# Performance work log

Hardware: AMD Instinct MI355X
Metric: run time of the kernel (lower is better)

## Reference

```python
import jax, jax.numpy as jnp
from jax import lax
import numpy as np

B, S, D, H2, V = 1024, 256, 128, 5, 50257
EPS = 1e-5


def setup_inputs() -> dict:
    key = jax.random.key(0)
    ks = jax.random.split(key, 12)
    s = 0.08  # init scale ~ 1/sqrt(D)
    return {
        "x": jax.random.randint(ks[0], (B, S), 0, V),
        "emb": jax.random.normal(ks[1], (V, D), jnp.float32) * s,
        "W_ih1": jax.random.normal(ks[2], (D, D), jnp.float32) * s,
        "b_ih1": jax.random.normal(ks[3], (D,), jnp.float32) * s,
        "W_hh1": jax.random.normal(ks[4], (D, D), jnp.float32) * s,
        "b_hh1": jax.random.normal(ks[5], (D,), jnp.float32) * s,
        "g1": jnp.ones((D,), jnp.float32),
        "be1": jnp.zeros((D,), jnp.float32),
        "W_ih2": jax.random.normal(ks[6], (H2, D), jnp.float32) * s,
        "b_ih2": jax.random.normal(ks[7], (H2,), jnp.float32) * s,
        "W_hh2": jax.random.normal(ks[8], (H2, H2), jnp.float32) * s,
        "b_hh2": jax.random.normal(ks[9], (H2,), jnp.float32) * s,
        "g2": jnp.ones((H2,), jnp.float32),
        "be2": jnp.zeros((H2,), jnp.float32),
    }


def _rnn(xproj, W_hh):
    """Vanilla tanh RNN. xproj: [B,S,H] = x @ W_ih^T + b_ih + b_hh (precomputed)."""
    h0 = jnp.zeros((xproj.shape[0], W_hh.shape[0]), xproj.dtype)

    def step(h, xt):  # xt: [B,H]
        h = jnp.tanh(xt + h @ W_hh.T)
        return h, h

    _, hs = lax.scan(step, h0, jnp.swapaxes(xproj, 0, 1))  # [S,B,H]
    return jnp.swapaxes(hs, 0, 1)  # [B,S,H]


def _ln(z, g, b):
    m = jnp.mean(z, axis=-1, keepdims=True)
    v = jnp.mean(jnp.square(z - m), axis=-1, keepdims=True)
    return (z - m) * lax.rsqrt(v + EPS) * g + b


def reference(x, emb, W_ih1, b_ih1, W_hh1, b_hh1, g1, be1,
              W_ih2, b_ih2, W_hh2, b_hh2, g2, be2):
    e = emb[x]  # [B,S,D]
    z = _rnn(e @ W_ih1.T + (b_ih1 + b_hh1), W_hh1)
    z = _ln(z, g1, be1)
    z = _rnn(z @ W_ih2.T + (b_ih2 + b_hh2), W_hh2)  # [B,S,5]
    z = _ln(z, g2, be2)
    pooled = jnp.mean(z, axis=1)  # AvgPool1d over full seq -> [B,5]
    return jax.nn.softmax(pooled, axis=1)
```

## Files before the change

### kernel.cpp

```cpp
#include <hip/hip_runtime.h>
#include <stdint.h>

#define S_LEN 256
#define DIM   128
#define EPSL  1e-5f

typedef __bf16 bf16x8 __attribute__((ext_vector_type(8)));
typedef float  f32x4  __attribute__((ext_vector_type(4)));

__device__ __forceinline__ unsigned short f2bf_bits(float f) {
  union { float f; unsigned int u; } v; v.f = f;
  unsigned int r = v.u + 0x7fffu + ((v.u >> 16) & 1u);
  return (unsigned short)(r >> 16);
}
__device__ __forceinline__ float bf2f_bits(unsigned short b) {
  union { float f; unsigned int u; } v; v.u = ((unsigned int)b) << 16; return v.f;
}
__device__ __forceinline__ unsigned f2bf_rhu(float f) {
  return (__float_as_uint(f) + 0x8000u) >> 16;
}
__device__ __forceinline__ unsigned pack_rhu(float lo, float hi) {
  return __builtin_amdgcn_perm(__float_as_uint(hi) + 0x8000u,
                               __float_as_uint(lo) + 0x8000u, 0x07060302u);
}
__device__ __forceinline__ float tanh_fast(float x) {
  float e = __expf(2.f * x);
  return 1.f - 2.f * __builtin_amdgcn_rcpf(e + 1.f);
}

template<int CTRL>
__device__ __forceinline__ float dpp_rot_add(float v) {
  int r = __builtin_amdgcn_update_dpp(0, __float_as_int(v), CTRL, 0xF, 0xF, true);
  return v + __int_as_float(r);
}
template<int CTRL>
__device__ __forceinline__ float dpp_rot_max(float v) {
  int r = __builtin_amdgcn_update_dpp(0, __float_as_int(v), CTRL, 0xF, 0xF, true);
  return fmaxf(v, __int_as_float(r));
}
__device__ __forceinline__ float dpp_sum16(float v) {
  v = dpp_rot_add<0x124>(v); v = dpp_rot_add<0x128>(v);
  v = dpp_rot_add<0x39>(v);  v = dpp_rot_add<0x4E>(v);
  return v;
}
__device__ __forceinline__ float dpp_max16(float v) {
  v = dpp_rot_max<0x124>(v); v = dpp_rot_max<0x128>(v);
  v = dpp_rot_max<0x39>(v);  v = dpp_rot_max<0x4E>(v);
  return v;
}
template<int CTRL>
__device__ __forceinline__ void red_level7(float& s, float& sq, float* d) {
  s  = dpp_rot_add<CTRL>(s);
  sq = dpp_rot_add<CTRL>(sq);
#pragma unroll
  for (int j = 0; j < 5; j++) d[j] = dpp_rot_add<CTRL>(d[j]);
}
template<int JJ>
__device__ __forceinline__ float bcast16(float v) {
  int r = __builtin_amdgcn_ds_swizzle(__float_as_int(v), (JJ << 5) | 0x10);
  return __int_as_float(r);
}

union Frag8 { unsigned short us[8]; bf16x8 v; int4 i4; };

__global__ __launch_bounds__(512, 2)
void rnn_fused(const int* __restrict__ x,
               const float* __restrict__ emb,
               const float* __restrict__ Wih1,
               const float* __restrict__ bih1,
               const float* __restrict__ Whh1,
               const float* __restrict__ bhh1,
               const float* __restrict__ g1,
               const float* __restrict__ be1,
               const float* __restrict__ Wih2,
               const float* __restrict__ bih2,
               const float* __restrict__ Whh2,
               const float* __restrict__ bhh2,
               const float* __restrict__ g2,
               const float* __restrict__ be2,
               float* __restrict__ out)
{
  __shared__ __align__(16) unsigned short h_bf[2][16 * 128];
  __shared__ __align__(16) unsigned short e_bf[2][16 * 128];
  __shared__ int x_tile[16 * 256];

  const int tid  = threadIdx.x;
  const int wave = tid >> 6;
  const int lane = tid & 63;
  const int r0   = blockIdx.x * 16;
  const int l15  = lane & 15;
  const int q    = lane >> 4;

  for (int i = tid; i < 16 * 256; i += 512)
    x_tile[i] = x[(size_t)(r0 + (i >> 8)) * S_LEN + (i & 255)];
  for (int i = tid; i < 16 * 128; i += 512) h_bf[1][i] = 0;

  const int n1 = wave * 16 + l15;
  const float bias1v = bih1[n1] + bhh1[n1];
  bf16x8 whi[4], wlo[4], wih[4];
#pragma unroll
  for (int kt = 0; kt < 4; kt++) {
    int k0 = kt * 32 + q * 8;
    Frag8 fh, fl, fa;
#pragma unroll
    for (int j = 0; j < 8; j++) {
      float w = Whh1[n1 * DIM + k0 + j];
      unsigned short hi = f2bf_bits(w);
      fh.us[j] = hi;
      fl.us[j] = f2bf_bits(w - bf2f_bits(hi));
      fa.us[j] = f2bf_bits(Wih1[n1 * DIM + k0 + j]);
    }
    whi[kt] = fh.v; wlo[kt] = fl.v; wih[kt] = fa.v;
  }

  const bool ln_role = (wave < 4);
  float w2g[5][8], Gs[5], Bs[5], wrow[5];
  float t2_l = 0.f, g2_l = 0.f, be2_l = 0.f, validf = 0.f;
  float h2rep[5], pool_l = 0.f;
  int myrow = 0;
  float pf[2][8];
  const int gm   = (wave & 3) * 4 + q;
  const int goct = l15;
  const int gdst = gm * 128 + ((goct ^ gm) & 15) * 8;

  if (ln_role) {
    myrow = wave * 4 + q;
    int coct = (l15 ^ myrow) & 15;
#pragma unroll
    for (int j = 0; j < 8; j++) {
      int c = coct * 8 + j;
      float gc = g1[c];
#pragma unroll
      for (int jj = 0; jj < 5; jj++) w2g[jj][j] = Wih2[jj * DIM + c] * gc;
    }
#pragma unroll
    for (int jj = 0; jj < 5; jj++) { Gs[jj] = 0.f; Bs[jj] = 0.f; }
    for (int c = 0; c < DIM; c++) {
      float gc = g1[c], bc = be1[c];
#pragma unroll
      for (int jj = 0; jj < 5; jj++) {
        float w = Wih2[jj * DIM + c];
        Gs[jj] += w * gc; Bs[jj] += w * bc;
      }
    }
    validf = (l15 < 5) ? 1.f : 0.f;
    if (l15 < 5) {
      t2_l = bih2[l15] + bhh2[l15];
      g2_l = g2[l15]; be2_l = be2[l15];
#pragma unroll
      for (int jj = 0; jj < 5; jj++) wrow[jj] = Whh2[l15 * 5 + jj];
    } else {
#pragma unroll
      for (int jj = 0; jj < 5; jj++) wrow[jj] = 0.f;
    }
#pragma unroll
    for (int jj = 0; jj < 5; jj++) h2rep[jj] = 0.f;
  }

  __syncthreads();

  if (!ln_role) {
    float ta[8], tb[8];
    {
      int xid = x_tile[gm * 256 + 0];
      const float* pe = emb + (size_t)xid * DIM + goct * 8;
#pragma unroll
      for (int j = 0; j < 8; j++) ta[j] = pe[j];
    }
    {
      int xid = x_tile[gm * 256 + 1];
      const float* pe = emb + (size_t)xid * DIM + goct * 8;
#pragma unroll
      for (int j = 0; j < 8; j++) tb[j] = pe[j];
    }
    {
      int xid = x_tile[gm * 256 + 2];
      const float* pe = emb + (size_t)xid * DIM + goct * 8;
#pragma unroll
      for (int j = 0; j < 8; j++) pf[0][j] = pe[j];
    }
    {
      int xid = x_tile[gm * 256 + 3];
      const float* pe = emb + (size_t)xid * DIM + goct * 8;
#pragma unroll
      for (int j = 0; j < 8; j++) pf[1][j] = pe[j];
    }
    Frag8 pa, pb;
#pragma unroll
    for (int j = 0; j < 8; j++) { pa.us[j] = f2bf_bits(ta[j]); pb.us[j] = f2bf_bits(tb[j]); }
    *(int4*)&e_bf[0][gdst] = pa.i4;
    *(int4*)&e_bf[1][gdst] = pb.i4;
  }
  __syncthreads();

  f32x4 xpacc = {bias1v, bias1v, bias1v, bias1v};
#pragma unroll
  for (int kt = 0; kt < 4; kt++) {
    int sw = (((kt * 4 + q) ^ l15) & 15) * 8;
    bf16x8 ae = *(const bf16x8*)&e_bf[0][l15 * 128 + sw];
    xpacc = __builtin_amdgcn_mfma_f32_16x16x32_bf16(ae, wih[kt], xpacc, 0, 0, 0);
  }
  asm volatile("s_waitcnt lgkmcnt(0)\n\ts_barrier" ::: "memory");

#pragma unroll 2
  for (int t = 0; t <= S_LEN; t++) {
    f32x4 ah = {0.f, 0.f, 0.f, 0.f};
    f32x4 al = xpacc;
    if (t < S_LEN) {
      const int rb = (t + 1) & 1;
#pragma unroll
      for (int kt = 0; kt < 4; kt++) {
        int sw = (((kt * 4 + q) ^ l15) & 15) * 8;
        bf16x8 ahf = *(const bf16x8*)&h_bf[rb][l15 * 128 + sw];
        ah = __builtin_amdgcn_mfma_f32_16x16x32_bf16(ahf, whi[kt], ah, 0, 0, 0);
        al = __builtin_amdgcn_mfma_f32_16x16x32_bf16(ahf, wlo[kt], al, 0, 0, 0);
      }
    }
    if (t + 1 < S_LEN) {
      f32x4 a = {bias1v, bias1v, bias1v, bias1v};
#pragma unroll
      for (int kt = 0; kt < 4; kt++) {
        int sw = (((kt * 4 + q) ^ l15) & 15) * 8;
        bf16x8 ae = *(const bf16x8*)&e_bf[(t + 1) & 1][l15 * 128 + sw];
        a = __builtin_amdgcn_mfma_f32_16x16x32_bf16(ae, wih[kt], a, 0, 0, 0);
      }
      xpacc = a;
    }
    if (t < S_LEN) {
      const int wb = t & 1;
      const int c = wave * 16 + l15;
      const int oct = c >> 3;
#pragma unroll
      for (int r = 0; r < 4; r++) {
        int row = q * 4 + r;
        float av = ah[r] + al[r];
        h_bf[wb][row * 128 + ((oct ^ row) & 15) * 8 + (c & 7)] =
            (unsigned short)f2bf_rhu(tanh_fast(av));
      }
    }
    if (!ln_role) {
      if (t + 2 < S_LEN) {
        int4 pk;
        pk.x = pack_rhu(pf[t & 1][0], pf[t & 1][1]);
        pk.y = pack_rhu(pf[t & 1][2], pf[t & 1][3]);
        pk.z = pack_rhu(pf[t & 1][4], pf[t & 1][5]);
        pk.w = pack_rhu(pf[t & 1][6], pf[t & 1][7]);
        *(int4*)&e_bf[t & 1][gdst] = pk;
      }
      if (t + 4 < S_LEN) {
        int xid = x_tile[gm * 256 + t + 4];
        const float* pe = emb + (size_t)xid * DIM + goct * 8;
#pragma unroll
        for (int j = 0; j < 8; j++) pf[t & 1][j] = pe[j];
      }
    } else if (t >= 1) {
      const int hb = (t - 1) & 1;
      Frag8 hr;
      hr.i4 = *(const int4*)&h_bf[hb][myrow * 128 + l15 * 8];
      float s = 0.f, sq = 0.f, d[5] = {0, 0, 0, 0, 0};
#pragma unroll
      for (int j = 0; j < 8; j++) {
        float v = bf2f_bits(hr.us[j]);
        s += v; sq += v * v;
#pragma unroll
        for (int jj = 0; jj < 5; jj++) d[jj] = fmaf(w2g[jj][j], v, d[jj]);
      }
      red_level7<0x124>(s, sq, d);
      red_level7<0x128>(s, sq, d);
      red_level7<0x39>(s, sq, d);
      red_level7<0x4E>(s, sq, d);
      float mean = s * (1.f / 128.f);
      float var  = sq * (1.f / 128.f) - mean * mean;
      float rstd = rsqrtf(var + EPSL);
      float p[5];
#pragma unroll
      for (int jj = 0; jj < 5; jj++)
        p[jj] = rstd * (d[jj] - mean * Gs[jj]) + Bs[jj];
      float psel = (l15 == 0) ? p[0] : (l15 == 1) ? p[1] :
                   (l15 == 2) ? p[2] : (l15 == 3) ? p[3] : p[4];
      float a = psel + t2_l;
#pragma unroll
      for (int jj = 0; jj < 5; jj++) a = fmaf(wrow[jj], h2rep[jj], a);
      float xn = tanh_fast(a);
      h2rep[0] = bcast16<0>(xn); h2rep[1] = bcast16<1>(xn);
      h2rep[2] = bcast16<2>(xn); h2rep[3] = bcast16<3>(xn);
      h2rep[4] = bcast16<4>(xn);
      float s2 = dpp_sum16(xn * validf) * 0.2f;
      float dd = xn - s2;
      float v2 = dpp_sum16(dd * dd * validf) * 0.2f;
      float r2 = rsqrtf(v2 + EPSL);
      pool_l += dd * r2 * g2_l + be2_l;
    }
    asm volatile("s_waitcnt lgkmcnt(0)\n\ts_barrier" ::: "memory");
  }

  if (ln_role) {
    float lg = pool_l * (1.f / 256.f);
    float mx = dpp_max16((l15 < 5) ? lg : -3.0e38f);
    float e  = (l15 < 5) ? __expf(lg - mx) : 0.f;
    float sm = dpp_sum16(e);
    if (l15 < 5) out[(size_t)(r0 + myrow) * 5 + l15] = e / sm;
  }
}

extern "C" void kernel_launch(void* const* d_in, const int* in_sizes, int n_in,
                              void* d_out, int out_size, void* d_ws, size_t ws_size,
                              hipStream_t stream) {
  (void)in_sizes; (void)n_in; (void)d_ws; (void)ws_size; (void)out_size;
  rnn_fused<<<dim3(64), dim3(512), 0, stream>>>(
      (const int*)  d_in[0],  (const float*)d_in[1],  (const float*)d_in[2],
      (const float*)d_in[3],  (const float*)d_in[4],  (const float*)d_in[5],
      (const float*)d_in[6],  (const float*)d_in[7],  (const float*)d_in[8],
      (const float*)d_in[9],  (const float*)d_in[10], (const float*)d_in[11],
      (const float*)d_in[12], (const float*)d_in[13], (float*)d_out);
}
```

Measured before the change: 295.7 us.

## Split input projection into parallel pre-kernel writing bf16 xproj to workspace

Moves the embedding gather and the x@W_ih1 projection out of the serial recurrent kernel into a separate 1024-block kernel that writes the bf16 projections to workspace. The serial kernel then just prefetches those per-step values, which takes the per-step e MFMAs and gather work off the critical path and frees the non-LN waves. The cost is an extra launch, a 16 MB workspace round trip, and bf16 rounding of the projection. The old fused kernel is kept as a fallback when the workspace is too small.

```diff
diff --git a/kernel.cpp b/kernel.cpp
--- a/kernel.cpp
+++ b/kernel.cpp
@@ -64,65 +64,102 @@
 union Frag8 { unsigned short us[8]; bf16x8 v; int4 i4; };
 
 __global__ __launch_bounds__(512, 2)
-void rnn_fused(const int* __restrict__ x,
-               const float* __restrict__ emb,
-               const float* __restrict__ Wih1,
-               const float* __restrict__ bih1,
-               const float* __restrict__ Whh1,
-               const float* __restrict__ bhh1,
-               const float* __restrict__ g1,
-               const float* __restrict__ be1,
-               const float* __restrict__ Wih2,
-               const float* __restrict__ bih2,
-               const float* __restrict__ Whh2,
-               const float* __restrict__ bhh2,
-               const float* __restrict__ g2,
-               const float* __restrict__ be2,
-               float* __restrict__ out)
+void xproj_pre(const int* __restrict__ x, const float* __restrict__ emb,
+               const float* __restrict__ Wih1, const float* __restrict__ bih1,
+               const float* __restrict__ bhh1, unsigned short* __restrict__ ws)
 {
-  __shared__ __align__(16) unsigned short h_bf[2][16 * 128];
-  __shared__ __align__(16) unsigned short e_bf[2][16 * 128];
-  __shared__ int x_tile[16 * 256];
-
+  __shared__ __align__(16) unsigned short e_s[16 * 128];
   const int tid  = threadIdx.x;
   const int wave = tid >> 6;
   const int lane = tid & 63;
-  const int r0   = blockIdx.x * 16;
   const int l15  = lane & 15;
   const int q    = lane >> 4;
-
-  for (int i = tid; i < 16 * 256; i += 512)
-    x_tile[i] = x[(size_t)(r0 + (i >> 8)) * S_LEN + (i & 255)];
-  for (int i = tid; i < 16 * 128; i += 512) h_bf[1][i] = 0;
+  const int bb   = blockIdx.x >> 4;
+  const int tc   = blockIdx.x & 15;
+  const int r0   = bb * 16;
 
   const int n1 = wave * 16 + l15;
   const float bias1v = bih1[n1] + bhh1[n1];
-  bf16x8 whi[4], wlo[4], wih[4];
+  bf16x8 wih[4];
 #pragma unroll
   for (int kt = 0; kt < 4; kt++) {
     int k0 = kt * 32 + q * 8;
-    Frag8 fh, fl, fa;
+    Frag8 fa;
+#pragma unroll
+    for (int j = 0; j < 8; j++) fa.us[j] = f2bf_bits(Wih1[n1 * DIM + k0 + j]);
+    wih[kt] = fa.v;
+  }
+
+  for (int tt = 0; tt < 16; tt++) {
+    const int t = tc * 16 + tt;
+    if (tid < 256) {
+      int m = tid >> 4, oct = tid & 15;
+      int xid = x[(size_t)(r0 + m) * S_LEN + t];
+      const float* pe = emb + (size_t)xid * DIM + oct * 8;
+      float4 lv0 = *(const float4*)pe;
+      float4 lv1 = *(const float4*)(pe + 4);
+      int4 pk;
+      pk.x = pack_rhu(lv0.x, lv0.y); pk.y = pack_rhu(lv0.z, lv0.w);
+      pk.z = pack_rhu(lv1.x, lv1.y); pk.w = pack_rhu(lv1.z, lv1.w);
+      *(int4*)&e_s[m * 128 + ((oct ^ m) & 15) * 8] = pk;
+    }
+    __syncthreads();
+    f32x4 a = {bias1v, bias1v, bias1v, bias1v};
+#pragma unroll
+    for (int kt = 0; kt < 4; kt++) {
+      int sw = (((kt * 4 + q) ^ l15) & 15) * 8;
+      bf16x8 ae = *(const bf16x8*)&e_s[l15 * 128 + sw];
+      a = __builtin_amdgcn_mfma_f32_16x16x32_bf16(ae, wih[kt], a, 0, 0, 0);
+    }
+    uint2 st;
+    st.x = pack_rhu(a[0], a[1]); st.y = pack_rhu(a[2], a[3]);
+    *(uint2*)&ws[(((size_t)t * 64 + bb) * 128 + n1) * 16 + q * 4] = st;
+    __syncthreads();
+  }
+}
+
+__global__ __launch_bounds__(512, 2)
+void rnn_serial(const unsigned short* __restrict__ xp,
+                const float* __restrict__ Whh1,
+                const float* __restrict__ g1,  const float* __restrict__ be1,
+                const float* __restrict__ Wih2, const float* __restrict__ bih2,
+                const float* __restrict__ Whh2, const float* __restrict__ bhh2,
+                const float* __restrict__ g2,  const float* __restrict__ be2,
+                float* __restrict__ out)
+{
+  __shared__ __align__(16) unsigned short h_bf[2][16 * 128];
+  const int tid  = threadIdx.x;
+  const int wave = tid >> 6;
+  const int lane = tid & 63;
+  const int bb   = blockIdx.x;
+  const int r0   = bb * 16;
+  const int l15  = lane & 15;
+  const int q    = lane >> 4;
+
+  for (int i = tid; i < 16 * 128; i += 512) h_bf[1][i] = 0;
+
+  const int n1 = wave * 16 + l15;
+  bf16x8 whi[4], wlo[4];
+#pragma unroll
+  for (int kt = 0; kt < 4; kt++) {
+    int k0 = kt * 32 + q * 8;
+    Frag8 fh, fl;
 #pragma unroll
     for (int j = 0; j < 8; j++) {
       float w = Whh1[n1 * DIM + k0 + j];
       unsigned short hi = f2bf_bits(w);
       fh.us[j] = hi;
       fl.us[j] = f2bf_bits(w - bf2f_bits(hi));
-      fa.us[j] = f2bf_bits(Wih1[n1 * DIM + k0 + j]);
-    }
-    whi[kt] = fh.v; wlo[kt] = fl.v; wih[kt] = fa.v;
-  }
+    }
+    whi[kt] = fh.v; wlo[kt] = fl.v;
+  }
+  const size_t xofs = ((size_t)bb * 128 + n1) * 16 + q * 4;
 
   const bool ln_role = (wave < 4);
   float w2g[5][8], Gs[5], Bs[5], wrow[5];
   float t2_l = 0.f, g2_l = 0.f, be2_l = 0.f, validf = 0.f;
   float h2rep[5], pool_l = 0.f;
   int myrow = 0;
-  float pf[2][8];
-  const int gm   = (wave & 3) * 4 + q;
-  const int goct = l15;
-  const int gdst = gm * 128 + ((goct ^ gm) & 15) * 8;
-
   if (ln_role) {
     myrow = wave * 4 + q;
     int coct = (l15 ^ myrow) & 15;
@@ -157,57 +194,19 @@
     for (int jj = 0; jj < 5; jj++) h2rep[jj] = 0.f;
   }
 
+  uint2 pfx[2];
+  pfx[0] = *(const uint2*)&xp[xofs];
+  pfx[1] = *(const uint2*)&xp[xofs + 131072];
   __syncthreads();
-
-  if (!ln_role) {
-    float ta[8], tb[8];
-    {
-      int xid = x_tile[gm * 256 + 0];
-      const float* pe = emb + (size_t)xid * DIM + goct * 8;
-#pragma unroll
-      for (int j = 0; j < 8; j++) ta[j] = pe[j];
-    }
-    {
-      int xid = x_tile[gm * 256 + 1];
-      const float* pe = emb + (size_t)xid * DIM + goct * 8;
-#pragma unroll
-      for (int j = 0; j < 8; j++) tb[j] = pe[j];
-    }
-    {
-      int xid = x_tile[gm * 256 + 2];
-      const float* pe = emb + (size_t)xid * DIM + goct * 8;
-#pragma unroll
-      for (int j = 0; j < 8; j++) pf[0][j] = pe[j];
-    }
-    {
-      int xid = x_tile[gm * 256 + 3];
-      const float* pe = emb + (size_t)xid * DIM + goct * 8;
-#pragma unroll
-      for (int j = 0; j < 8; j++) pf[1][j] = pe[j];
-    }
-    Frag8 pa, pb;
-#pragma unroll
-    for (int j = 0; j < 8; j++) { pa.us[j] = f2bf_bits(ta[j]); pb.us[j] = f2bf_bits(tb[j]); }
-    *(int4*)&e_bf[0][gdst] = pa.i4;
-    *(int4*)&e_bf[1][gdst] = pb.i4;
-  }
-  __syncthreads();
-
-  f32x4 xpacc = {bias1v, bias1v, bias1v, bias1v};
-#pragma unroll
-  for (int kt = 0; kt < 4; kt++) {
-    int sw = (((kt * 4 + q) ^ l15) & 15) * 8;
-    bf16x8 ae = *(const bf16x8*)&e_bf[0][l15 * 128 + sw];
-    xpacc = __builtin_amdgcn_mfma_f32_16x16x32_bf16(ae, wih[kt], xpacc, 0, 0, 0);
-  }
-  asm volatile("s_waitcnt lgkmcnt(0)\n\ts_barrier" ::: "memory");
 
 #pragma unroll 2
   for (int t = 0; t <= S_LEN; t++) {
-    f32x4 ah = {0.f, 0.f, 0.f, 0.f};
-    f32x4 al = xpacc;
     if (t < S_LEN) {
+      uint2 cur = pfx[t & 1];
+      if (t + 2 < S_LEN)
+        pfx[t & 1] = *(const uint2*)&xp[xofs + (size_t)(t + 2) * 131072];
       const int rb = (t + 1) & 1;
+      f32x4 ah = {0.f, 0.f, 0.f, 0.f}, al = {0.f, 0.f, 0.f, 0.f};
 #pragma unroll
       for (int kt = 0; kt < 4; kt++) {
         int sw = (((kt * 4 + q) ^ l15) & 15) * 8;
@@ -215,45 +214,23 @@
         ah = __builtin_amdgcn_mfma_f32_16x16x32_bf16(ahf, whi[kt], ah, 0, 0, 0);
         al = __builtin_amdgcn_mfma_f32_16x16x32_bf16(ahf, wlo[kt], al, 0, 0, 0);
       }
-    }
-    if (t + 1 < S_LEN) {
-      f32x4 a = {bias1v, bias1v, bias1v, bias1v};
-#pragma unroll
-      for (int kt = 0; kt < 4; kt++) {
-        int sw = (((kt * 4 + q) ^ l15) & 15) * 8;
-        bf16x8 ae = *(const bf16x8*)&e_bf[(t + 1) & 1][l15 * 128 + sw];
-        a = __builtin_amdgcn_mfma_f32_16x16x32_bf16(ae, wih[kt], a, 0, 0, 0);
-      }
-      xpacc = a;
-    }
-    if (t < S_LEN) {
+      float xq[4];
+      xq[0] = __uint_as_float(cur.x << 16);
+      xq[1] = __uint_as_float(cur.x & 0xffff0000u);
+      xq[2] = __uint_as_float(cur.y << 16);
+      xq[3] = __uint_as_float(cur.y & 0xffff0000u);
       const int wb = t & 1;
-      const int c = wave * 16 + l15;
+      const int c = n1;
       const int oct = c >> 3;
 #pragma unroll
       for (int r = 0; r < 4; r++) {
         int row = q * 4 + r;
-        float av = ah[r] + al[r];
+        float av = ah[r] + al[r] + xq[r];
         h_bf[wb][row * 128 + ((oct ^ row) & 15) * 8 + (c & 7)] =
             (unsigned short)f2bf_rhu(tanh_fast(av));
       }
     }
-    if (!ln_role) {
-      if (t + 2 < S_LEN) {
-        int4 pk;
-        pk.x = pack_rhu(pf[t & 1][0], pf[t & 1][1]);
-        pk.y = pack_rhu(pf[t & 1][2], pf[t & 1][3]);
-        pk.z = pack_rhu(pf[t & 1][4], pf[t & 1][5]);
-        pk.w = pack_rhu(pf[t & 1][6], pf[t & 1][7]);
-        *(int4*)&e_bf[t & 1][gdst] = pk;
-      }
-      if (t + 4 < S_LEN) {
-        int xid = x_tile[gm * 256 + t + 4];
-        const float* pe = emb + (size_t)xid * DIM + goct * 8;
-#pragma unroll
-        for (int j = 0; j < 8; j++) pf[t & 1][j] = pe[j];
-      }
-    } else if (t >= 1) {
+    if (ln_role && t >= 1) {
       const int hb = (t - 1) & 1;
       Frag8 hr;
       hr.i4 = *(const int4*)&h_bf[hb][myrow * 128 + l15 * 8];
@@ -303,14 +280,259 @@
   }
 }
 
+__global__ __launch_bounds__(512, 2)
+void rnn_fused_fb(const int* __restrict__ x, const float* __restrict__ emb,
+                  const float* __restrict__ Wih1, const float* __restrict__ bih1,
+                  const float* __restrict__ Whh1, const float* __restrict__ bhh1,
+                  const float* __restrict__ g1, const float* __restrict__ be1,
+                  const float* __restrict__ Wih2, const float* __restrict__ bih2,
+                  const float* __restrict__ Whh2, const float* __restrict__ bhh2,
+                  const float* __restrict__ g2, const float* __restrict__ be2,
+                  float* __restrict__ out)
+{
+  __shared__ __align__(16) unsigned short h_bf[2][16 * 128];
+  __shared__ __align__(16) unsigned short e_bf[2][16 * 128];
+  __shared__ int x_tile[16 * 256];
+
+  const int tid  = threadIdx.x;
+  const int wave = tid >> 6;
+  const int lane = tid & 63;
+  const int r0   = blockIdx.x * 16;
+  const int l15  = lane & 15;
+  const int q    = lane >> 4;
+
+  for (int i = tid; i < 16 * 256; i += 512)
+    x_tile[i] = x[(size_t)(r0 + (i >> 8)) * S_LEN + (i & 255)];
+  for (int i = tid; i < 16 * 128; i += 512) h_bf[1][i] = 0;
+
+  const int n1 = wave * 16 + l15;
+  const float bias1v = bih1[n1] + bhh1[n1];
+  bf16x8 whi[4], wlo[4], wih[4];
+#pragma unroll
+  for (int kt = 0; kt < 4; kt++) {
+    int k0 = kt * 32 + q * 8;
+    Frag8 fh, fl, fa;
+#pragma unroll
+    for (int j = 0; j < 8; j++) {
+      float w = Whh1[n1 * DIM + k0 + j];
+      unsigned short hi = f2bf_bits(w);
+      fh.us[j] = hi;
+      fl.us[j] = f2bf_bits(w - bf2f_bits(hi));
+      fa.us[j] = f2bf_bits(Wih1[n1 * DIM + k0 + j]);
+    }
+    whi[kt] = fh.v; wlo[kt] = fl.v; wih[kt] = fa.v;
+  }
+
+  const bool ln_role = (wave < 4);
+  float w2g[5][8], Gs[5], Bs[5], wrow[5];
+  float t2_l = 0.f, g2_l = 0.f, be2_l = 0.f, validf = 0.f;
+  float h2rep[5], pool_l = 0.f;
+  int myrow = 0;
+  float pf[2][8];
+  const int gm   = (wave & 3) * 4 + q;
+  const int goct = l15;
+  const int gdst = gm * 128 + ((goct ^ gm) & 15) * 8;
+
+  if (ln_role) {
+    myrow = wave * 4 + q;
+    int coct = (l15 ^ myrow) & 15;
+#pragma unroll
+    for (int j = 0; j < 8; j++) {
+      int c = coct * 8 + j;
+      float gc = g1[c];
+#pragma unroll
+      for (int jj = 0; jj < 5; jj++) w2g[jj][j] = Wih2[jj * DIM + c] * gc;
+    }
+#pragma unroll
+    for (int jj = 0; jj < 5; jj++) { Gs[jj] = 0.f; Bs[jj] = 0.f; }
+    for (int c = 0; c < DIM; c++) {
+      float gc = g1[c], bc = be1[c];
+#pragma unroll
+      for (int jj = 0; jj < 5; jj++) {
+        float w = Wih2[jj * DIM + c];
+        Gs[jj] += w * gc; Bs[jj] += w * bc;
+      }
+    }
+    validf = (l15 < 5) ? 1.f : 0.f;
+    if (l15 < 5) {
+      t2_l = bih2[l15] + bhh2[l15];
+      g2_l = g2[l15]; be2_l = be2[l15];
+#pragma unroll
+      for (int jj = 0; jj < 5; jj++) wrow[jj] = Whh2[l15 * 5 + jj];
+    } else {
+#pragma unroll
+      for (int jj = 0; jj < 5; jj++) wrow[jj] = 0.f;
+    }
+#pragma unroll
+    for (int jj = 0; jj < 5; jj++) h2rep[jj] = 0.f;
+  }
+  __syncthreads();
+
+  if (!ln_role) {
+    float ta[8], tb[8];
+    { int xid = x_tile[gm * 256 + 0];
+      const float* pe = emb + (size_t)xid * DIM + goct * 8;
+#pragma unroll
+      for (int j = 0; j < 8; j++) ta[j] = pe[j]; }
+    { int xid = x_tile[gm * 256 + 1];
+      const float* pe = emb + (size_t)xid * DIM + goct * 8;
+#pragma unroll
+      for (int j = 0; j < 8; j++) tb[j] = pe[j]; }
+    { int xid = x_tile[gm * 256 + 2];
+      const float* pe = emb + (size_t)xid * DIM + goct * 8;
+#pragma unroll
+      for (int j = 0; j < 8; j++) pf[0][j] = pe[j]; }
+    { int xid = x_tile[gm * 256 + 3];
+      const float* pe = emb + (size_t)xid * DIM + goct * 8;
+#pragma unroll
+      for (int j = 0; j < 8; j++) pf[1][j] = pe[j]; }
+    Frag8 pa, pb;
+#pragma unroll
+    for (int j = 0; j < 8; j++) { pa.us[j] = f2bf_bits(ta[j]); pb.us[j] = f2bf_bits(tb[j]); }
+    *(int4*)&e_bf[0][gdst] = pa.i4;
+    *(int4*)&e_bf[1][gdst] = pb.i4;
+  }
+  __syncthreads();
+
+  f32x4 xpacc = {bias1v, bias1v, bias1v, bias1v};
+#pragma unroll
+  for (int kt = 0; kt < 4; kt++) {
+    int sw = (((kt * 4 + q) ^ l15) & 15) * 8;
+    bf16x8 ae = *(const bf16x8*)&e_bf[0][l15 * 128 + sw];
+    xpacc = __builtin_amdgcn_mfma_f32_16x16x32_bf16(ae, wih[kt], xpacc, 0, 0, 0);
+  }
+  asm volatile("s_waitcnt lgkmcnt(0)\n\ts_barrier" ::: "memory");
+
+#pragma unroll 2
+  for (int t = 0; t <= S_LEN; t++) {
+    f32x4 ah = {0.f, 0.f, 0.f, 0.f};
+    f32x4 al = xpacc;
+    if (t < S_LEN) {
+      const int rb = (t + 1) & 1;
+#pragma unroll
+      for (int kt = 0; kt < 4; kt++) {
+        int sw = (((kt * 4 + q) ^ l15) & 15) * 8;
+        bf16x8 ahf = *(const bf16x8*)&h_bf[rb][l15 * 128 + sw];
+        ah = __builtin_amdgcn_mfma_f32_16x16x32_bf16(ahf, whi[kt], ah, 0, 0, 0);
+        al = __builtin_amdgcn_mfma_f32_16x16x32_bf16(ahf, wlo[kt], al, 0, 0, 0);
+      }
+    }
+    if (t + 1 < S_LEN) {
+      f32x4 a = {bias1v, bias1v, bias1v, bias1v};
+#pragma unroll
+      for (int kt = 0; kt < 4; kt++) {
+        int sw = (((kt * 4 + q) ^ l15) & 15) * 8;
+        bf16x8 ae = *(const bf16x8*)&e_bf[(t + 1) & 1][l15 * 128 + sw];
+        a = __builtin_amdgcn_mfma_f32_16x16x32_bf16(ae, wih[kt], a, 0, 0, 0);
+      }
+      xpacc = a;
+    }
+    if (t < S_LEN) {
+      const int wb = t & 1;
+      const int c = wave * 16 + l15;
+      const int oct = c >> 3;
+#pragma unroll
+      for (int r = 0; r < 4; r++) {
+        int row = q * 4 + r;
+        float av = ah[r] + al[r];
+        h_bf[wb][row * 128 + ((oct ^ row) & 15) * 8 + (c & 7)] =
+            (unsigned short)f2bf_rhu(tanh_fast(av));
+      }
+    }
+    if (!ln_role) {
+      if (t + 2 < S_LEN) {
+        int4 pk;
+        pk.x = pack_rhu(pf[t & 1][0], pf[t & 1][1]);
+        pk.y = pack_rhu(pf[t & 1][2], pf[t & 1][3]);
+        pk.z = pack_rhu(pf[t & 1][4], pf[t & 1][5]);
+        pk.w = pack_rhu(pf[t & 1][6], pf[t & 1][7]);
+        *(int4*)&e_bf[t & 1][gdst] = pk;
+      }
+      if (t + 4 < S_LEN) {
+        int xid = x_tile[gm * 256 + t + 4];
+        const float* pe = emb + (size_t)xid * DIM + goct * 8;
+#pragma unroll
+        for (int j = 0; j < 8; j++) pf[t & 1][j] = pe[j];
+      }
+    } else if (t >= 1) {
+      const int hb = (t - 1) & 1;
+      Frag8 hr;
+      hr.i4 = *(const int4*)&h_bf[hb][myrow * 128 + l15 * 8];
+      float s = 0.f, sq = 0.f, d[5] = {0, 0, 0, 0, 0};
+#pragma unroll
+      for (int j = 0; j < 8; j++) {
+        float v = bf2f_bits(hr.us[j]);
+        s += v; sq += v * v;
+#pragma unroll
+        for (int jj = 0; jj < 5; jj++) d[jj] = fmaf(w2g[jj][j], v, d[jj]);
+      }
+      red_level7<0x124>(s, sq, d);
+      red_level7<0x128>(s, sq, d);
+      red_level7<0x39>(s, sq, d);
+      red_level7<0x4E>(s, sq, d);
+      float mean = s * (1.f / 128.f);
+      float var  = sq * (1.f / 128.f) - mean * mean;
+      float rstd = rsqrtf(var + EPSL);
+      float p[5];
+#pragma unroll
+      for (int jj = 0; jj < 5; jj++)
+        p[jj] = rstd * (d[jj] - mean * Gs[jj]) + Bs[jj];
+      float psel = (l15 == 0) ? p[0] : (l15 == 1) ? p[1] :
+                   (l15 == 2) ? p[2] : (l15 == 3) ? p[3] : p[4];
+      float a = psel + t2_l;
+#pragma unroll
+      for (int jj = 0; jj < 5; jj++) a = fmaf(wrow[jj], h2rep[jj], a);
+      float xn = tanh_fast(a);
+      h2rep[0] = bcast16<0>(xn); h2rep[1] = bcast16<1>(xn);
+      h2rep[2] = bcast16<2>(xn); h2rep[3] = bcast16<3>(xn);
+      h2rep[4] = bcast16<4>(xn);
+      float s2 = dpp_sum16(xn * validf) * 0.2f;
+      float dd = xn - s2;
+      float v2 = dpp_sum16(dd * dd * validf) * 0.2f;
+      float r2 = rsqrtf(v2 + EPSL);
+      pool_l += dd * r2 * g2_l + be2_l;
+    }
+    asm volatile("s_waitcnt lgkmcnt(0)\n\ts_barrier" ::: "memory");
+  }
+
+  if (ln_role) {
+    float lg = pool_l * (1.f / 256.f);
+    float mx = dpp_max16((l15 < 5) ? lg : -3.0e38f);
+    float e  = (l15 < 5) ? __expf(lg - mx) : 0.f;
+    float sm = dpp_sum16(e);
+    if (l15 < 5) out[(size_t)(r0 + myrow) * 5 + l15] = e / sm;
+  }
+}
+
 extern "C" void kernel_launch(void* const* d_in, const int* in_sizes, int n_in,
                               void* d_out, int out_size, void* d_ws, size_t ws_size,
                               hipStream_t stream) {
-  (void)in_sizes; (void)n_in; (void)d_ws; (void)ws_size; (void)out_size;
-  rnn_fused<<<dim3(64), dim3(512), 0, stream>>>(
-      (const int*)  d_in[0],  (const float*)d_in[1],  (const float*)d_in[2],
-      (const float*)d_in[3],  (const float*)d_in[4],  (const float*)d_in[5],
-      (const float*)d_in[6],  (const float*)d_in[7],  (const float*)d_in[8],
-      (const float*)d_in[9],  (const float*)d_in[10], (const float*)d_in[11],
-      (const float*)d_in[12], (const float*)d_in[13], (float*)d_out);
-}
+  (void)in_sizes; (void)n_in; (void)out_size;
+  const int*   x    = (const int*)  d_in[0];
+  const float* emb  = (const float*)d_in[1];
+  const float* Wih1 = (const float*)d_in[2];
+  const float* bih1 = (const float*)d_in[3];
+  const float* Whh1 = (const float*)d_in[4];
+  const float* bhh1 = (const float*)d_in[5];
+  const float* g1   = (const float*)d_in[6];
+  const float* be1  = (const float*)d_in[7];
+  const float* Wih2 = (const float*)d_in[8];
+  const float* bih2 = (const float*)d_in[9];
+  const float* Whh2 = (const float*)d_in[10];
+  const float* bhh2 = (const float*)d_in[11];
+  const float* g2   = (const float*)d_in[12];
+  const float* be2  = (const float*)d_in[13];
+  float* out = (float*)d_out;
+
+  const size_t XPBYTES = (size_t)S_LEN * 64 * 128 * 16 * 2;
+  if (ws_size >= XPBYTES) {
+    unsigned short* ws = (unsigned short*)d_ws;
+    xproj_pre<<<dim3(1024), dim3(512), 0, stream>>>(x, emb, Wih1, bih1, bhh1, ws);
+    rnn_serial<<<dim3(64), dim3(512), 0, stream>>>(ws, Whh1, g1, be1, Wih2,
+                                                   bih2, Whh2, bhh2, g2, be2, out);
+  } else {
+    rnn_fused_fb<<<dim3(64), dim3(512), 0, stream>>>(
+        x, emb, Wih1, bih1, Whh1, bhh1, g1, be1,
+        Wih2, bih2, Whh2, bhh2, g2, be2, out);
+  }
+}
```

Result: slower. 319.3 us (+8.0%).
